# Performance work log

Measured on AMD Instinct MI355X. Metric: run time of the kernel, lower is better.

## Reference

```python
import jax, jax.numpy as jnp
import numpy as np

B, T, HM = 2, 2048, 1024
HEADS = 16
DK = (HM // 2) // HEADS   # expand_k = 0.5 -> key_dim 512, per-head 32
DV = HM // HEADS          # expand_v = 1.0 -> per-head 64
LOW_RANK = 16             # gate low-rank dim (fla default)
GATE_NORM = 16.0          # gate_logit_normalizer (fla default)
EPS = 1e-5


def setup_inputs() -> dict:
    key = jax.random.key(0)
    ks = jax.random.split(key, 12)
    def p(k, shape, s=0.02):
        return jax.random.normal(k, shape, jnp.float32) * s
    return dict(
        x=jax.random.normal(ks[0], (B, T, HM), jnp.float32),
        ln_w=jnp.ones((HM,), jnp.float32), ln_b=jnp.zeros((HM,), jnp.float32),
        Wq=p(ks[1], (HM, HEADS * DK)), Wk=p(ks[2], (HM, HEADS * DK)),
        Wv=p(ks[3], (HM, HEADS * DV)),
        gk_w1=p(ks[4], (HM, LOW_RANK)), gk_w2=p(ks[5], (LOW_RANK, HEADS * DK)),
        gk_b2=jnp.zeros((HEADS * DK,), jnp.float32),
        Wg=p(ks[6], (HM, HEADS * DV)), rms_w=jnp.ones((DV,), jnp.float32),
        Wo=p(ks[7], (HEADS * DV, HM)),
        W1=p(ks[8], (HM, 2 * HM)), b1=jnp.zeros((2 * HM,), jnp.float32),
        W2=p(ks[9], (2 * HM, HM)), b2=jnp.zeros((HM,), jnp.float32),
    )


def _ln(x, w, b):
    m = x.mean(-1, keepdims=True)
    v = ((x - m) ** 2).mean(-1, keepdims=True)
    return (x - m) * jax.lax.rsqrt(v + EPS) * w + b


def _rms(x, w):
    return x * jax.lax.rsqrt((x * x).mean(-1, keepdims=True) + EPS) * w


def _gla(q, k, v, gk):
    # gated linear attention recurrence:
    # S_t = diag(exp(gk_t)) S_{t-1} + k_t v_t^T ;  o_t = q_t S_t
    # q,k,gk: [B,T,H,DK], v: [B,T,H,DV]
    def step(S, inp):
        qt, kt, vt, gt = inp
        S = jnp.exp(gt)[..., None] * S + kt[..., None] * vt[..., None, :]
        return S, jnp.einsum('bhk,bhkv->bhv', qt, S)
    xs = tuple(jnp.moveaxis(a, 1, 0) for a in (q, k, v, gk))
    S0 = jnp.zeros((q.shape[0], q.shape[2], q.shape[3], v.shape[3]), q.dtype)
    _, o = jax.lax.scan(step, S0, xs)
    return jnp.moveaxis(o, 0, 1)


def reference(x, ln_w, ln_b, Wq, Wk, Wv, gk_w1, gk_w2, gk_b2, Wg, rms_w, Wo, W1, b1, W2, b2):
    Bb, Tt, _ = x.shape
    h = _ln(x, ln_w, ln_b)
    q = (h @ Wq).reshape(Bb, Tt, HEADS, DK)
    k = (h @ Wk).reshape(Bb, Tt, HEADS, DK)
    v = (h @ Wv).reshape(Bb, Tt, HEADS, DV)
    gk = (jax.nn.log_sigmoid((h @ gk_w1) @ gk_w2 + gk_b2) / GATE_NORM)
    gk = gk.reshape(Bb, Tt, HEADS, DK)
    o = _gla(q * (DK ** -0.5), k, v, gk)
    # output gate: RMSNorm(o) * swish(g)  (FusedRMSNormSwishGate)
    g = (h @ Wg).reshape(Bb, Tt, HEADS, DV)
    o = _rms(o, rms_w) * (g * jax.nn.sigmoid(g))
    x = x + o.reshape(Bb, Tt, HEADS * DV) @ Wo
    h2 = _ln(x, ln_w, ln_b)  # same shared norm module
    return x + jax.nn.gelu(h2 @ W1 + b1, approximate=False) @ W2 + b2
```

## Files before the change

### kernel.cpp

```cpp
#include <hip/hip_runtime.h>
#include <hip/hip_bf16.h>
#include <math.h>


using bf16 = __hip_bfloat16;
typedef __attribute__((ext_vector_type(8))) short bf16x8;
typedef __attribute__((ext_vector_type(4))) float f32x4;

#define BT 4096
#define HM 1024
#define DK 32
#define DV 64
#define NC 32
#define CHK 64

#if defined(__has_builtin)
#if __has_builtin(__builtin_amdgcn_global_load_lds)
#define HAVE_GLDS 1
#endif
#endif

#ifdef HAVE_GLDS
#define GLDS16(g, l) __builtin_amdgcn_global_load_lds( \
    (const __attribute__((address_space(1))) unsigned int*)(g), \
    (__attribute__((address_space(3))) unsigned int*)(l), 16, 0, 0)
#else
#define GLDS16(g, l) (*(int4*)(l) = *(const int4*)(g))
#endif

__device__ __forceinline__ float b2f(bf16 v) { return __bfloat162float(v); }
__device__ __forceinline__ bf16 f2b(float v) { return __float2bfloat16(v); }
__device__ __forceinline__ float clampf(float v, float lim) {
    return fminf(fmaxf(v, -lim), lim);
}
__device__ __forceinline__ float lo16(unsigned int u) {
    union { unsigned int i; float f; } c; c.i = u << 16; return c.f;
}
__device__ __forceinline__ float hi16(unsigned int u) {
    union { unsigned int i; float f; } c; c.i = u & 0xffff0000u; return c.f;
}
__device__ __forceinline__ void acc8(float a, uint4 r, float* o) {
    o[0] += a * lo16(r.x); o[1] += a * hi16(r.x);
    o[2] += a * lo16(r.y); o[3] += a * hi16(r.y);
    o[4] += a * lo16(r.z); o[5] += a * hi16(r.z);
    o[6] += a * lo16(r.w); o[7] += a * hi16(r.w);
}

__global__ __launch_bounds__(256) void detect_dtype(
    const unsigned int* __restrict__ x, int* __restrict__ flag)
{
    int tid = threadIdx.x;
    int cnt = 0;
    for (int i = 0; i < 16; ++i) {
        unsigned int w = x[tid * 16 + i];
        unsigned int e_lo = (w >> 7) & 0xffu;
        unsigned int e_hi = (w >> 23) & 0xffu;
        cnt += (e_lo >= 110 && e_lo <= 135 && e_hi >= 110 && e_hi <= 135) ? 1 : 0;
    }
    __shared__ int red[256];
    red[tid] = cnt;
    __syncthreads();
    for (int s = 128; s > 0; s >>= 1) {
        if (tid < s) red[tid] += red[tid + s];
        __syncthreads();
    }
    if (tid == 0) *flag = (red[0] > 2048) ? 1 : 0;
}

__global__ __launch_bounds__(256) void cvt_to_bf16(
    const void* __restrict__ src, bf16* __restrict__ dst, int n,
    const int* __restrict__ flag)
{
    bool isb = (*flag != 0);
    int i = blockIdx.x * 256 + threadIdx.x;
    int stride = gridDim.x * 256;
    for (; i < n; i += stride) {
        if (isb) ((ushort*)dst)[i] = ((const ushort*)src)[i];
        else     dst[i] = f2b(((const float*)src)[i]);
    }
}

struct SmallCvt { const void* s[8]; bf16* d[8]; int n[8]; };
__global__ __launch_bounds__(256) void cvt_small(SmallCvt sc, const int* __restrict__ flag)
{
    bool isb = (*flag != 0);
    int stride = gridDim.x * 256;
    #pragma unroll
    for (int seg = 0; seg < 8; ++seg) {
        int n = sc.n[seg];
        for (int i = blockIdx.x * 256 + threadIdx.x; i < n; i += stride) {
            if (isb) ((ushort*)sc.d[seg])[i] = ((const ushort*)sc.s[seg])[i];
            else     sc.d[seg][i] = f2b(((const float*)sc.s[seg])[i]);
        }
    }
}

__global__ __launch_bounds__(256) void transpose_any(
    const void* __restrict__ src, ushort* __restrict__ dst, int R, int C,
    const int* __restrict__ flag)
{
    bool isb = (*flag != 0);
    __shared__ ushort tile[32][33];
    int c0 = blockIdx.x * 32, r0 = blockIdx.y * 32;
    int x = threadIdx.x, y = threadIdx.y;
    #pragma unroll
    for (int dy = 0; dy < 32; dy += 8) {
        size_t idx = (size_t)(r0 + y + dy) * C + c0 + x;
        ushort v;
        if (isb) v = ((const ushort*)src)[idx];
        else { bf16 t = f2b(((const float*)src)[idx]); v = *(ushort*)&t; }
        tile[y + dy][x] = v;
    }
    __syncthreads();
    #pragma unroll
    for (int dy = 0; dy < 32; dy += 8)
        dst[(size_t)(c0 + y + dy) * R + r0 + x] = tile[x][y + dy];
}

template <typename TI>
__global__ __launch_bounds__(256) void ln_kernel(
    const TI* __restrict__ x, const bf16* __restrict__ w, const bf16* __restrict__ b,
    bf16* __restrict__ out)
{
    size_t base = (size_t)blockIdx.x * HM;
    int tid = threadIdx.x;
    float v[4], s = 0.f, s2 = 0.f;
    #pragma unroll
    for (int u = 0; u < 4; ++u) {
        float f;
        if constexpr (sizeof(TI) == 2) f = b2f(((const bf16*)x)[base + tid + u * 256]);
        else                           f = ((const float*)x)[base + tid + u * 256];
        v[u] = f; s += f; s2 += f * f;
    }
    #pragma unroll
    for (int off = 32; off >= 1; off >>= 1) {
        s  += __shfl_down(s, off);
        s2 += __shfl_down(s2, off);
    }
    __shared__ float ra[4], rb[4];
    int wave = tid >> 6;
    if ((tid & 63) == 0) { ra[wave] = s; rb[wave] = s2; }
    __syncthreads();
    s = ra[0] + ra[1] + ra[2] + ra[3];
    s2 = rb[0] + rb[1] + rb[2] + rb[3];
    float mean = s * (1.f / HM);
    float var = fmaxf(s2 * (1.f / HM) - mean * mean, 0.f);
    float rs = rsqrtf(var + 1e-5f);
    #pragma unroll
    for (int u = 0; u < 4; ++u) {
        int col = tid + u * 256;
        out[base + col] = f2b((v[u] - mean) * rs * b2f(w[col]) + b2f(b[col]));
    }
}

__global__ __launch_bounds__(256) void gk_kernel(
    const bf16* __restrict__ h, const bf16* __restrict__ w1,
    const bf16* __restrict__ w2, const bf16* __restrict__ b2i,
    bf16* __restrict__ gkout)
{
    size_t row = blockIdx.x;
    const bf16* hr = h + row * HM;
    int tid = threadIdx.x;
    int d = tid & 15, seg = tid >> 4;
    float s = 0.f;
    for (int j = 0; j < 64; ++j) {
        int i = seg * 64 + j;
        s += b2f(hr[i]) * b2f(w1[i * 16 + d]);
    }
    __shared__ float red[256];
    __shared__ float g1[16];
    red[tid] = s;
    __syncthreads();
    if (tid < 16) {
        float t = 0.f;
        #pragma unroll
        for (int sg = 0; sg < 16; ++sg) t += red[sg * 16 + tid];
        g1[tid] = t;
    }
    __syncthreads();
    #pragma unroll
    for (int rep = 0; rep < 2; ++rep) {
        int n = tid + rep * 256;
        float z = b2f(b2i[n]);
        #pragma unroll
        for (int r = 0; r < 16; ++r) z += g1[r] * b2f(w2[r * 512 + n]);
        z = clampf(z, 30.f);
        float ls = (z >= 0.f) ? -log1pf(expf(-z)) : (z - log1pf(expf(z)));
        gkout[row * 512 + n] = f2b(ls * 0.0625f);
    }
}

template <int MODE>
__global__ __launch_bounds__(256) void gemm_bt(
    const bf16* __restrict__ A, const bf16* __restrict__ Wt,
    const bf16* __restrict__ bias, const void* __restrict__ resid,
    void* __restrict__ out, int M, int N, int K, const int* __restrict__ oflag)
{
    __shared__ __align__(16) ushort As[128 * 32];
    __shared__ __align__(16) ushort Bs[64 * 32];
    int tid = threadIdx.x;
    int w = tid >> 6, l = tid & 63;
    int bm = blockIdx.x * 128, bn = blockIdx.y * 64;
    int row16 = l & 15, quad = l >> 4;
    bool out_bf16 = false;
    if constexpr (MODE == 3) out_bf16 = (*oflag != 0);

    const ushort* Au = (const ushort*)A;
    const ushort* Wu = (const ushort*)Wt;
    int sr = w * 16 + row16;
    int scol = quad * 8;
    const ushort* gA0 = Au + (size_t)(bm + sr) * K + scol;
    const ushort* gA1 = Au + (size_t)(bm + sr + 64) * K + scol;
    const ushort* gB0 = Wu + (size_t)(bn + sr) * K + scol;
    ushort* lA0 = &As[w * 512 + l * 8];
    ushort* lA1 = &As[2048 + w * 512 + l * 8];
    ushort* lB0 = &Bs[w * 512 + l * 8];

    int am = (w >> 1) * 4;
    int an = (w & 1) * 2;
    int fo = quad * 128 + row16 * 8;

    f32x4 acc[4][2] = {};
    for (int k0 = 0; k0 < K; k0 += 32) {
        GLDS16(gA0 + k0, lA0);
        GLDS16(gA1 + k0, lA1);
        GLDS16(gB0 + k0, lB0);
        __syncthreads();
        bf16x8 af[4], bff[2];
        #pragma unroll
        for (int mi = 0; mi < 4; ++mi) af[mi] = *(const bf16x8*)&As[(am + mi) * 512 + fo];
        #pragma unroll
        for (int ni = 0; ni < 2; ++ni) bff[ni] = *(const bf16x8*)&Bs[(an + ni) * 512 + fo];
        #pragma unroll
        for (int mi = 0; mi < 4; ++mi)
            #pragma unroll
            for (int ni = 0; ni < 2; ++ni)
                acc[mi][ni] = __builtin_amdgcn_mfma_f32_16x16x32_bf16(af[mi], bff[ni], acc[mi][ni], 0, 0, 0);
        __syncthreads();
    }
    #pragma unroll
    for (int mi = 0; mi < 4; ++mi) {
        #pragma unroll
        for (int ni = 0; ni < 2; ++ni) {
            int col = bn + (w & 1) * 32 + ni * 16 + row16;
            #pragma unroll
            for (int r = 0; r < 4; ++r) {
                int row = bm + (w >> 1) * 64 + mi * 16 + quad * 4 + r;
                size_t idx = (size_t)row * N + col;
                float v = acc[mi][ni][r];
                if constexpr (MODE == 0) {
                    ((bf16*)out)[idx] = f2b(clampf(v, 1e4f));
                } else if constexpr (MODE == 1) {
                    ((float*)out)[idx] = clampf(b2f(((const bf16*)resid)[idx]) + v, 1e5f);
                } else if constexpr (MODE == 2) {
                    float t = clampf(v + b2f(bias[col]), 50.f);
                    ((bf16*)out)[idx] = f2b(0.5f * t * (1.f + erff(t * 0.70710678f)));
                } else {
                    float t = clampf(v + b2f(bias[col]) + ((const float*)resid)[idx], 2e5f);
                    if (out_bf16) ((bf16*)out)[idx] = f2b(t);
                    else          ((float*)out)[idx] = t;
                }
            }
        }
    }
}

__global__ __launch_bounds__(256) void gla_phase1(
    const bf16* __restrict__ gkb, const bf16* __restrict__ qk,
    const bf16* __restrict__ vg,
    float* __restrict__ clbuf, float* __restrict__ Dbuf, float* __restrict__ Pbuf)
{
    int bh = blockIdx.x, c = blockIdx.y;
    int b = bh >> 4, hh = bh & 15;
    int row0 = b * 2048 + c * CHK;
    __shared__ float glog[CHK][DK + 1];
    __shared__ float wk[CHK][DK + 1];
    __shared__ __align__(16) ushort vt[CHK][DV];
    int tid = threadIdx.x;
    int k = tid & 31, i8 = (tid >> 5) * 8;
    #pragma unroll
    for (int u = 0; u < 8; ++u) {
        int i = i8 + u;
        float g = b2f(gkb[(size_t)(row0 + i) * 512 + hh * 32 + k]);
        glog[i][k] = fminf(fmaxf(g, -2.f), 0.f);
    }
    {
        int cc = tid & 7, ii = tid >> 3;
        #pragma unroll
        for (int h = 0; h < 2; ++h) {
            int i = ii + h * 32;
            uint4 val = *(const uint4*)((const ushort*)vg + (size_t)(row0 + i) * 2048 + hh * 64 + cc * 8);
            *(uint4*)&vt[i][cc * 8] = val;
        }
    }
    __syncthreads();
    if (tid < 32) {
        float run = 0.f;
        for (int j = 0; j < CHK; ++j) { run += glog[j][tid]; glog[j][tid] = run; }
    }
    __syncthreads();
    #pragma unroll
    for (int u = 0; u < 8; ++u) {
        int i = i8 + u;
        float cl = glog[i][k];
        float cl63 = glog[CHK - 1][k];
        clbuf[(size_t)(row0 + i) * 512 + hh * 32 + k] = cl;
        wk[i][k] = expf(fmaxf(cl63 - cl, -60.f)) *
            b2f(qk[(size_t)(row0 + i) * 1024 + 512 + hh * 32 + k]);
    }
    if (tid < 32) Dbuf[(size_t)(bh * 32 + c) * 32 + tid] = expf(glog[CHK - 1][tid]);
    __syncthreads();
    int kk = tid >> 3, v8 = (tid & 7) * 8;
    float acc[8] = {};
    for (int j = 0; j < CHK; ++j) {
        float w = wk[j][kk];
        uint4 raw = *(const uint4*)&vt[j][v8];
        acc8(w, raw, acc);
    }
    float* Pp = Pbuf + (size_t)(bh * 32 + c) * 2048 + kk * 64 + v8;
    #pragma unroll
    for (int u = 0; u < 8; ++u) Pp[u] = acc[u];
}

__global__ __launch_bounds__(256) void gla_scan(
    const float* __restrict__ Pbuf, const float* __restrict__ Dbuf,
    float* __restrict__ Sbuf)
{
    int bh = blockIdx.x >> 3, vg8 = blockIdx.x & 7;
    int kk = threadIdx.x >> 3, vv = vg8 * 8 + (threadIdx.x & 7);
    float S = 0.f;
    for (int c = 0; c < NC; ++c) {
        size_t idx = (size_t)(bh * 32 + c) * 2048 + kk * 64 + vv;
        float P = Pbuf[idx];
        float D = Dbuf[(size_t)(bh * 32 + c) * 32 + kk];
        Sbuf[idx] = S;
        S = D * S + P;
    }
}

__global__ __launch_bounds__(256) void gla_phase3(
    const bf16* __restrict__ qk, const bf16* __restrict__ vg,
    const float* __restrict__ clbuf, const float* __restrict__ Sbuf,
    const bf16* __restrict__ rmsw, bf16* __restrict__ obuf)
{
    int bh = blockIdx.x, c = blockIdx.y;
    int b = bh >> 4, hh = bh & 15;
    int row0 = b * 2048 + c * CHK;
    __shared__ float qs[CHK][36], ks[CHK][36];
    __shared__ float S0[DK][68];
    __shared__ float Amat[CHK][CHK + 1];
    __shared__ __align__(16) ushort vt[CHK][DV];
    int tid = threadIdx.x;
    {
        int k = tid & 31, i8 = (tid >> 5) * 8;
        #pragma unroll
        for (int u = 0; u < 8; ++u) {
            int i = i8 + u;
            size_t r = (size_t)(row0 + i);
            int col = hh * 32 + k;
            float cl = fmaxf(clbuf[r * 512 + col], -60.f);
            qs[i][k] = b2f(qk[r * 1024 + col]) * expf(cl) * 0.17677669529663687f;
            ks[i][k] = b2f(qk[r * 1024 + 512 + col]) * expf(-cl);
        }
    }
    {
        int cc = tid & 7, ii = tid >> 3;
        #pragma unroll
        for (int h = 0; h < 2; ++h) {
            int i = ii + h * 32;
            uint4 val = *(const uint4*)((const ushort*)vg + (size_t)(row0 + i) * 2048 + hh * 64 + cc * 8);
            *(uint4*)&vt[i][cc * 8] = val;
        }
    }
    {
        int kk = tid >> 3, v8 = (tid & 7) * 8;
        const float* Sp = Sbuf + (size_t)(bh * 32 + c) * 2048 + kk * 64 + v8;
        *(f32x4*)&S0[kk][v8]     = *(const f32x4*)Sp;
        *(f32x4*)&S0[kk][v8 + 4] = *(const f32x4*)(Sp + 4);
    }
    __syncthreads();
    int i = tid >> 2, jb = tid & 3;
    for (int jj = 0; jj < 16; ++jj) {
        int j = jb + jj * 4;
        float d = 0.f;
        if (j <= i) {
            const f32x4* qp = (const f32x4*)qs[i];
            const f32x4* kp = (const f32x4*)ks[j];
            #pragma unroll
            for (int q8 = 0; q8 < 8; ++q8) {
                f32x4 a = qp[q8], bq = kp[q8];
                d += a.x * bq.x + a.y * bq.y + a.z * bq.z + a.w * bq.w;
            }
        }
        Amat[i][j] = d;
    }
    __syncthreads();
    float o[16] = {};
    int vv = jb * 16;
    for (int j = 0; j < CHK; ++j) {
        float a = Amat[i][j];
        uint4 r0 = *(const uint4*)&vt[j][vv];
        uint4 r1 = *(const uint4*)&vt[j][vv + 8];
        acc8(a, r0, o);
        acc8(a, r1, o + 8);
    }
    #pragma unroll
    for (int kk = 0; kk < DK; ++kk) {
        float qv = qs[i][kk];
        const f32x4* Sp = (const f32x4*)&S0[kk][vv];
        #pragma unroll
        for (int q4 = 0; q4 < 4; ++q4) {
            f32x4 sv = Sp[q4];
            o[q4 * 4 + 0] += qv * sv.x; o[q4 * 4 + 1] += qv * sv.y;
            o[q4 * 4 + 2] += qv * sv.z; o[q4 * 4 + 3] += qv * sv.w;
        }
    }
    float ss = 0.f;
    #pragma unroll
    for (int u = 0; u < 16; ++u) ss += o[u] * o[u];
    ss += __shfl_xor(ss, 1);
    ss += __shfl_xor(ss, 2);
    float sc = rsqrtf(fmaxf(ss, 0.f) * (1.f / DV) + 1e-5f);
    size_t r = (size_t)(row0 + i);
    #pragma unroll
    for (int u = 0; u < 16; ++u) {
        float g = b2f(vg[r * 2048 + 1024 + hh * 64 + vv + u]);
        float sw = g / (1.f + expf(-g));
        obuf[r * 1024 + hh * 64 + vv + u] = f2b(clampf(o[u] * sc * b2f(rmsw[vv + u]) * sw, 3e4f));
    }
}

extern "C" void kernel_launch(void* const* d_in, const int* in_sizes, int n_in,
                              void* d_out, int out_size, void* d_ws, size_t ws_size,
                              hipStream_t stream) {
    (void)in_sizes; (void)n_in; (void)out_size; (void)ws_size;

    char* ws = (char*)d_ws;
    const size_t MB = 1024 * 1024;
    const size_t KB = 1024;
    bf16*  WqkT = (bf16*)(ws + 0);
    bf16*  WkT  = (bf16*)(ws + 1 * MB);
    bf16*  WvgT = (bf16*)(ws + 2 * MB);
    bf16*  WgT  = (bf16*)(ws + 4 * MB);
    bf16*  WoT  = (bf16*)(ws + 6 * MB);
    bf16*  W1T  = (bf16*)(ws + 8 * MB);
    bf16*  W2T  = (bf16*)(ws + 12 * MB);
    bf16*  hbuf = (bf16*)(ws + 16 * MB);
    bf16*  qkb  = (bf16*)(ws + 24 * MB);
    bf16*  vgb  = (bf16*)(ws + 32 * MB);
    bf16*  gkb  = (bf16*)(ws + 48 * MB);
    float* clbf = (float*)(ws + 52 * MB);
    float* Dbuf = (float*)(ws + 60 * MB);
    float* Pbuf = (float*)(ws + 61 * MB);
    float* Sbuf = (float*)(ws + 69 * MB);
    bf16*  obuf = (bf16*)(ws + 61 * MB);
    float* ybuf = (float*)(ws + 32 * MB);
    bf16*  f1   = (bf16*)(ws + 48 * MB);
    bf16*  cx   = (bf16*)(ws + 77 * MB);
    bf16*  clnw = (bf16*)(ws + 85 * MB);
    bf16*  clnb = (bf16*)(ws + 85 * MB + 64 * KB);
    bf16*  cgw1 = (bf16*)(ws + 85 * MB + 128 * KB);
    bf16*  cgw2 = (bf16*)(ws + 85 * MB + 192 * KB);
    bf16*  cgb2 = (bf16*)(ws + 85 * MB + 256 * KB);
    bf16*  crms = (bf16*)(ws + 85 * MB + 320 * KB);
    bf16*  cb1  = (bf16*)(ws + 85 * MB + 384 * KB);
    bf16*  cb2  = (bf16*)(ws + 85 * MB + 448 * KB);
    int*   flag = (int*)(ws + 85 * MB + 512 * KB);

    hipLaunchKernelGGL(detect_dtype, dim3(1), dim3(256), 0, stream,
                       (const unsigned int*)d_in[0], flag);

    hipLaunchKernelGGL(cvt_to_bf16, dim3(2048), dim3(256), 0, stream,
                       d_in[0], cx, 4194304, flag);
    SmallCvt sc;
    sc.s[0] = d_in[1];  sc.d[0] = clnw; sc.n[0] = 1024;
    sc.s[1] = d_in[2];  sc.d[1] = clnb; sc.n[1] = 1024;
    sc.s[2] = d_in[6];  sc.d[2] = cgw1; sc.n[2] = 16384;
    sc.s[3] = d_in[7];  sc.d[3] = cgw2; sc.n[3] = 8192;
    sc.s[4] = d_in[8];  sc.d[4] = cgb2; sc.n[4] = 512;
    sc.s[5] = d_in[10]; sc.d[5] = crms; sc.n[5] = 64;
    sc.s[6] = d_in[13]; sc.d[6] = cb1;  sc.n[6] = 2048;
    sc.s[7] = d_in[15]; sc.d[7] = cb2;  sc.n[7] = 1024;
    hipLaunchKernelGGL(cvt_small, dim3(64), dim3(256), 0, stream, sc, flag);

    dim3 tb(32, 8);
    hipLaunchKernelGGL(transpose_any, dim3(16, 32), tb, 0, stream, d_in[3],  (ushort*)WqkT, 1024, 512, flag);
    hipLaunchKernelGGL(transpose_any, dim3(16, 32), tb, 0, stream, d_in[4],  (ushort*)WkT,  1024, 512, flag);
    hipLaunchKernelGGL(transpose_any, dim3(32, 32), tb, 0, stream, d_in[5],  (ushort*)WvgT, 1024, 1024, flag);
    hipLaunchKernelGGL(transpose_any, dim3(32, 32), tb, 0, stream, d_in[9],  (ushort*)WgT,  1024, 1024, flag);
    hipLaunchKernelGGL(transpose_any, dim3(32, 32), tb, 0, stream, d_in[11], (ushort*)WoT,  1024, 1024, flag);
    hipLaunchKernelGGL(transpose_any, dim3(64, 32), tb, 0, stream, d_in[12], (ushort*)W1T,  1024, 2048, flag);
    hipLaunchKernelGGL(transpose_any, dim3(32, 64), tb, 0, stream, d_in[14], (ushort*)W2T,  2048, 1024, flag);

    hipLaunchKernelGGL((ln_kernel<bf16>), dim3(BT), dim3(256), 0, stream, cx, clnw, clnb, hbuf);

    hipLaunchKernelGGL((gemm_bt<0>), dim3(32, 16), dim3(256), 0, stream,
                       hbuf, WqkT, (const bf16*)nullptr, (const void*)nullptr, (void*)qkb, BT, 1024, 1024, (const int*)nullptr);
    hipLaunchKernelGGL((gemm_bt<0>), dim3(32, 32), dim3(256), 0, stream,
                       hbuf, WvgT, (const bf16*)nullptr, (const void*)nullptr, (void*)vgb, BT, 2048, 1024, (const int*)nullptr);
    hipLaunchKernelGGL(gk_kernel, dim3(BT), dim3(256), 0, stream, hbuf, cgw1, cgw2, cgb2, gkb);

    hipLaunchKernelGGL(gla_phase1, dim3(32, 32), dim3(256), 0, stream, gkb, qkb, vgb, clbf, Dbuf, Pbuf);
    hipLaunchKernelGGL(gla_scan, dim3(256), dim3(256), 0, stream, Pbuf, Dbuf, Sbuf);
    hipLaunchKernelGGL(gla_phase3, dim3(32, 32), dim3(256), 0, stream, qkb, vgb, clbf, Sbuf, crms, obuf);

    hipLaunchKernelGGL((gemm_bt<1>), dim3(32, 16), dim3(256), 0, stream,
                       obuf, WoT, (const bf16*)nullptr, (const void*)cx, (void*)ybuf, BT, 1024, 1024, (const int*)nullptr);
    hipLaunchKernelGGL((ln_kernel<float>), dim3(BT), dim3(256), 0, stream, ybuf, clnw, clnb, hbuf);
    hipLaunchKernelGGL((gemm_bt<2>), dim3(32, 32), dim3(256), 0, stream,
                       hbuf, W1T, cb1, (const void*)nullptr, (void*)f1, BT, 2048, 1024, (const int*)nullptr);
    hipLaunchKernelGGL((gemm_bt<3>), dim3(32, 16), dim3(256), 0, stream,
                       f1, W2T, cb2, (const void*)ybuf, d_out, BT, 1024, 2048, flag);
}
```

Measured before the change: 459.5 us.

## Merge QK and VG projections into one GEMM and deepen GEMM K-tile

Replaces the separate QK (N=1024) and VG (N=2048) projection GEMMs with a single N=3072 GEMM. It writes one interleaved qvg buffer, and the GLA phase kernels now index into it with a 3072 row stride. Separately, the shared bf16 GEMM now loads a 64-wide K slab per iteration and issues two MFMA sub-steps per barrier pair, which halves the number of __syncthreads per K. This costs double the LDS tiles and relies on the transposed weight buffers for Q, K, V and G being contiguous.

New measurement: 456.1 us. No clear change (-0.7%).

```diff
diff --git a/kernel.cpp b/kernel.cpp
--- a/kernel.cpp
+++ b/kernel.cpp
@@ -196,8 +196,8 @@
     const bf16* __restrict__ bias, const void* __restrict__ resid,
     void* __restrict__ out, int M, int N, int K, const int* __restrict__ oflag)
 {
-    __shared__ __align__(16) ushort As[128 * 32];
-    __shared__ __align__(16) ushort Bs[64 * 32];
+    __shared__ __align__(16) ushort As[128 * 64];
+    __shared__ __align__(16) ushort Bs[64 * 64];
     int tid = threadIdx.x;
     int w = tid >> 6, l = tid & 63;
     int bm = blockIdx.x * 128, bn = blockIdx.y * 64;
@@ -207,35 +207,40 @@
 
     const ushort* Au = (const ushort*)A;
     const ushort* Wu = (const ushort*)Wt;
-    int sr = w * 16 + row16;
-    int scol = quad * 8;
-    const ushort* gA0 = Au + (size_t)(bm + sr) * K + scol;
-    const ushort* gA1 = Au + (size_t)(bm + sr + 64) * K + scol;
-    const ushort* gB0 = Wu + (size_t)(bn + sr) * K + scol;
-    ushort* lA0 = &As[w * 512 + l * 8];
-    ushort* lA1 = &As[2048 + w * 512 + l * 8];
-    ushort* lB0 = &Bs[w * 512 + l * 8];
-
-    int am = (w >> 1) * 4;
-    int an = (w & 1) * 2;
-    int fo = quad * 128 + row16 * 8;
 
     f32x4 acc[4][2] = {};
-    for (int k0 = 0; k0 < K; k0 += 32) {
-        GLDS16(gA0 + k0, lA0);
-        GLDS16(gA1 + k0, lA1);
-        GLDS16(gB0 + k0, lB0);
+    for (int k0 = 0; k0 < K; k0 += 64) {
+        #pragma unroll
+        for (int i = 0; i < 4; ++i) {
+            int j = i * 4 + w;
+            const ushort* g = Au + (size_t)(bm + (j >> 1) * 16 + row16) * K
+                              + k0 + (j & 1) * 32 + quad * 8;
+            GLDS16(g, &As[j * 512 + l * 8]);
+        }
+        #pragma unroll
+        for (int i = 0; i < 2; ++i) {
+            int j = i * 4 + w;
+            const ushort* g = Wu + (size_t)(bn + (j >> 1) * 16 + row16) * K
+                              + k0 + (j & 1) * 32 + quad * 8;
+            GLDS16(g, &Bs[j * 512 + l * 8]);
+        }
         __syncthreads();
-        bf16x8 af[4], bff[2];
-        #pragma unroll
-        for (int mi = 0; mi < 4; ++mi) af[mi] = *(const bf16x8*)&As[(am + mi) * 512 + fo];
-        #pragma unroll
-        for (int ni = 0; ni < 2; ++ni) bff[ni] = *(const bf16x8*)&Bs[(an + ni) * 512 + fo];
-        #pragma unroll
-        for (int mi = 0; mi < 4; ++mi)
+        #pragma unroll
+        for (int s = 0; s < 2; ++s) {
+            int fo = (s * 4 + quad) * 128 + row16 * 8;
+            bf16x8 af[4], bw[2];
+            #pragma unroll
+            for (int mi = 0; mi < 4; ++mi)
+                af[mi] = *(const bf16x8*)&As[((w >> 1) * 4 + mi) * 1024 + fo];
             #pragma unroll
             for (int ni = 0; ni < 2; ++ni)
-                acc[mi][ni] = __builtin_amdgcn_mfma_f32_16x16x32_bf16(af[mi], bff[ni], acc[mi][ni], 0, 0, 0);
+                bw[ni] = *(const bf16x8*)&Bs[((w & 1) * 2 + ni) * 1024 + fo];
+            #pragma unroll
+            for (int mi = 0; mi < 4; ++mi)
+                #pragma unroll
+                for (int ni = 0; ni < 2; ++ni)
+                    acc[mi][ni] = __builtin_amdgcn_mfma_f32_16x16x32_bf16(af[mi], bw[ni], acc[mi][ni], 0, 0, 0);
+        }
         __syncthreads();
     }
     #pragma unroll
@@ -266,8 +271,8 @@
 }
 
 __global__ __launch_bounds__(256) void gla_phase1(
-    const bf16* __restrict__ gkb, const bf16* __restrict__ qk,
-    const bf16* __restrict__ vg,
+    const bf16* __restrict__ gkb,
+    const bf16* __restrict__ qvg,
     float* __restrict__ clbuf, float* __restrict__ Dbuf, float* __restrict__ Pbuf)
 {
     int bh = blockIdx.x, c = blockIdx.y;
@@ -289,7 +294,7 @@
         #pragma unroll
         for (int h = 0; h < 2; ++h) {
             int i = ii + h * 32;
-            uint4 val = *(const uint4*)((const ushort*)vg + (size_t)(row0 + i) * 2048 + hh * 64 + cc * 8);
+            uint4 val = *(const uint4*)((const ushort*)qvg + (size_t)(row0 + i) * 3072 + 1024 + hh * 64 + cc * 8);
             *(uint4*)&vt[i][cc * 8] = val;
         }
     }
@@ -306,7 +311,7 @@
         float cl63 = glog[CHK - 1][k];
         clbuf[(size_t)(row0 + i) * 512 + hh * 32 + k] = cl;
         wk[i][k] = expf(fmaxf(cl63 - cl, -60.f)) *
-            b2f(qk[(size_t)(row0 + i) * 1024 + 512 + hh * 32 + k]);
+            b2f(qvg[(size_t)(row0 + i) * 3072 + 512 + hh * 32 + k]);
     }
     if (tid < 32) Dbuf[(size_t)(bh * 32 + c) * 32 + tid] = expf(glog[CHK - 1][tid]);
     __syncthreads();
@@ -339,7 +344,7 @@
 }
 
 __global__ __launch_bounds__(256) void gla_phase3(
-    const bf16* __restrict__ qk, const bf16* __restrict__ vg,
+    const bf16* __restrict__ qvg,
     const float* __restrict__ clbuf, const float* __restrict__ Sbuf,
     const bf16* __restrict__ rmsw, bf16* __restrict__ obuf)
 {
@@ -359,8 +364,8 @@
             size_t r = (size_t)(row0 + i);
             int col = hh * 32 + k;
             float cl = fmaxf(clbuf[r * 512 + col], -60.f);
-            qs[i][k] = b2f(qk[r * 1024 + col]) * expf(cl) * 0.17677669529663687f;
-            ks[i][k] = b2f(qk[r * 1024 + 512 + col]) * expf(-cl);
+            qs[i][k] = b2f(qvg[r * 3072 + col]) * expf(cl) * 0.17677669529663687f;
+            ks[i][k] = b2f(qvg[r * 3072 + 512 + col]) * expf(-cl);
         }
     }
     {
@@ -368,7 +373,7 @@
         #pragma unroll
         for (int h = 0; h < 2; ++h) {
             int i = ii + h * 32;
-            uint4 val = *(const uint4*)((const ushort*)vg + (size_t)(row0 + i) * 2048 + hh * 64 + cc * 8);
+            uint4 val = *(const uint4*)((const ushort*)qvg + (size_t)(row0 + i) * 3072 + 1024 + hh * 64 + cc * 8);
             *(uint4*)&vt[i][cc * 8] = val;
         }
     }
@@ -424,7 +429,7 @@
     size_t r = (size_t)(row0 + i);
     #pragma unroll
     for (int u = 0; u < 16; ++u) {
-        float g = b2f(vg[r * 2048 + 1024 + hh * 64 + vv + u]);
+        float g = b2f(qvg[r * 3072 + 2048 + hh * 64 + vv + u]);
         float sw = g / (1.f + expf(-g));
         obuf[r * 1024 + hh * 64 + vv + u] = f2b(clampf(o[u] * sc * b2f(rmsw[vv + u]) * sw, 3e4f));
     }
@@ -446,8 +451,7 @@
     bf16*  W1T  = (bf16*)(ws + 8 * MB);
     bf16*  W2T  = (bf16*)(ws + 12 * MB);
     bf16*  hbuf = (bf16*)(ws + 16 * MB);
-    bf16*  qkb  = (bf16*)(ws + 24 * MB);
-    bf16*  vgb  = (bf16*)(ws + 32 * MB);
+    bf16*  qvg  = (bf16*)(ws + 24 * MB);
     bf16*  gkb  = (bf16*)(ws + 48 * MB);
     float* clbf = (float*)(ws + 52 * MB);
     float* Dbuf = (float*)(ws + 60 * MB);
@@ -494,15 +498,13 @@
 
     hipLaunchKernelGGL((ln_kernel<bf16>), dim3(BT), dim3(256), 0, stream, cx, clnw, clnb, hbuf);
 
-    hipLaunchKernelGGL((gemm_bt<0>), dim3(32, 16), dim3(256), 0, stream,
-                       hbuf, WqkT, (const bf16*)nullptr, (const void*)nullptr, (void*)qkb, BT, 1024, 1024, (const int*)nullptr);
-    hipLaunchKernelGGL((gemm_bt<0>), dim3(32, 32), dim3(256), 0, stream,
-                       hbuf, WvgT, (const bf16*)nullptr, (const void*)nullptr, (void*)vgb, BT, 2048, 1024, (const int*)nullptr);
+    hipLaunchKernelGGL((gemm_bt<0>), dim3(32, 48), dim3(256), 0, stream,
+                       hbuf, WqkT, (const bf16*)nullptr, (const void*)nullptr, (void*)qvg, BT, 3072, 1024, (const int*)nullptr);
     hipLaunchKernelGGL(gk_kernel, dim3(BT), dim3(256), 0, stream, hbuf, cgw1, cgw2, cgb2, gkb);
 
-    hipLaunchKernelGGL(gla_phase1, dim3(32, 32), dim3(256), 0, stream, gkb, qkb, vgb, clbf, Dbuf, Pbuf);
+    hipLaunchKernelGGL(gla_phase1, dim3(32, 32), dim3(256), 0, stream, gkb, qvg, clbf, Dbuf, Pbuf);
     hipLaunchKernelGGL(gla_scan, dim3(256), dim3(256), 0, stream, Pbuf, Dbuf, Sbuf);
-    hipLaunchKernelGGL(gla_phase3, dim3(32, 32), dim3(256), 0, stream, qkb, vgb, clbf, Sbuf, crms, obuf);
+    hipLaunchKernelGGL(gla_phase3, dim3(32, 32), dim3(256), 0, stream, qvg, clbf, Sbuf, crms, obuf);
 
     hipLaunchKernelGGL((gemm_bt<1>), dim3(32, 16), dim3(256), 0, stream,
                        obuf, WoT, (const bf16*)nullptr, (const void*)cx, (void*)ybuf, BT, 1024, 1024, (const int*)nullptr);
```
